# Performance work log

Hardware: AMD Instinct MI355X
Metric: run time of the kernel (lower is better)

The kernel has to match this reference:

```python
import jax, jax.numpy as jnp
import numpy as np

B, L, E, D = 4, 4096, 768, 64

def setup_inputs() -> dict:
    key = jax.random.key(0)
    ks = jax.random.split(key, 7)
    x = jax.random.normal(ks[0], (B, L, E), dtype=jnp.float32)
    # True = masked (strict upper triangle), as in masked_fill semantics
    causal_mask = jnp.triu(jnp.ones((L, L), dtype=bool), k=1)
    # True = valid token (inverted with ~ inside forward); all valid to avoid NaN rows
    pad_mask = jnp.ones((B, L), dtype=bool)
    s = 1.0 / np.sqrt(E)
    Wk = jax.random.uniform(ks[1], (E, D), jnp.float32, -s, s)
    bk = jax.random.uniform(ks[2], (D,), jnp.float32, -s, s)
    Wq = jax.random.uniform(ks[3], (E, D), jnp.float32, -s, s)
    bq = jax.random.uniform(ks[4], (D,), jnp.float32, -s, s)
    Wv = jax.random.uniform(ks[5], (E, D), jnp.float32, -s, s)
    bv = jax.random.uniform(ks[6], (D,), jnp.float32, -s, s)
    return {"x": x, "causal_mask": causal_mask, "pad_mask": pad_mask,
            "Wk": Wk, "bk": bk, "Wq": Wq, "bq": bq, "Wv": Wv, "bv": bv}

def reference(x, causal_mask, pad_mask, Wk, bk, Wq, bq, Wv, bv):
    # Linear projections: [B,L,E] @ [E,D] + [D]
    K = jnp.einsum('ble,ed->bld', x, Wk) + bk
    Q = jnp.einsum('ble,ed->bld', x, Wq) + bq
    V = jnp.einsum('ble,ed->bld', x, Wv) + bv
    d = Q.shape[-1]
    scores = jnp.einsum('bqd,bkd->bqk', Q, K) / jnp.sqrt(jnp.asarray(d, Q.dtype))
    # full_mask: causal (True=masked) OR key-position padding (~pad_mask, broadcast over query dim)
    full_mask = causal_mask[None, :, :] | (~pad_mask)[:, None, :]
    scores = jnp.where(full_mask, -jnp.inf, scores)
    attn = jax.nn.softmax(scores, axis=-1)
    out = jnp.einsum('bqk,bkd->bqd', attn, V)
    return out
```

## Files before the change

### kernel.cpp

```cpp
#include <hip/hip_runtime.h>

#define L_SEQ 4096
#define BATCH 4
#define EDIM 768

typedef __attribute__((ext_vector_type(8))) short bf16x8;
typedef __attribute__((ext_vector_type(4))) float f32x4;
typedef __attribute__((ext_vector_type(4))) unsigned short u16x4;
typedef __attribute__((ext_vector_type(8))) unsigned short u16x8;
typedef __attribute__((ext_vector_type(4))) _Float16 f16x4;
typedef __attribute__((ext_vector_type(8))) _Float16 f16x8;

__device__ __forceinline__ unsigned short f2bf(float f) {
  unsigned u = __builtin_bit_cast(unsigned, f);
  u += 0x7FFFu + ((u >> 16) & 1u);
  return (unsigned short)(u >> 16);
}

__global__ __launch_bounds__(256) void prep_kernel(
    const float* __restrict__ Wq, const float* __restrict__ Wk,
    const float* __restrict__ Wv, unsigned short* __restrict__ WT) {
  int g = blockIdx.x * 256 + threadIdx.x;
  if (g >= 192 * EDIM) return;
  int row = g / EDIM, k = g - row * EDIM;
  int z = row >> 6, n = row & 63;
  const float* W = (z == 0) ? Wq : (z == 1) ? Wk : Wv;
  WT[g] = f2bf(W[k * 64 + n]);
}

__global__ __launch_bounds__(256) void proj_kernel(
    const float* __restrict__ x, const unsigned short* __restrict__ WT,
    const float* __restrict__ bq, const float* __restrict__ bk, const float* __restrict__ bv,
    unsigned short* __restrict__ Qo, unsigned short* __restrict__ Kf,
    _Float16* __restrict__ Vf) {
  __shared__ unsigned short SH[2 * 13824];
  int tid = threadIdx.x;
  int w = tid >> 6, lane = tid & 63, l15 = lane & 15, g4 = lane >> 4;
  int m0 = blockIdx.x * 64;
  int brow = tid >> 3, bsg = tid & 7;

  f32x4 acc[3][4];
#pragma unroll
  for (int z = 0; z < 3; z++)
#pragma unroll
    for (int cf = 0; cf < 4; cf++) acc[z][cf] = (f32x4){0.f, 0.f, 0.f, 0.f};

  f32x4 arA[4], arB[4];
  u16x8 brA[6], brB[6];

  auto loadA = [&](f32x4 (&ar)[4], int k0) {
    const float* xp = x + (size_t)(m0 + 16 * w + l15) * EDIM + k0 + g4 * 8;
    ar[0] = *(const f32x4*)xp;
    ar[1] = *(const f32x4*)(xp + 4);
    ar[2] = *(const f32x4*)(xp + 32);
    ar[3] = *(const f32x4*)(xp + 36);
  };
  auto loadB = [&](u16x8 (&br)[6], int k0) {
#pragma unroll
    for (int pp = 0; pp < 6; pp++)
      br[pp] = *(const u16x8*)(WT + (size_t)(brow + pp * 32) * EDIM + k0 + bsg * 8);
  };
  auto writeB = [&](int cur, u16x8 (&br)[6]) {
#pragma unroll
    for (int pp = 0; pp < 6; pp++)
      *(u16x8*)&SH[cur * 13824 + (brow + pp * 32) * 72 + bsg * 8] = br[pp];
  };
  auto mkfrag = [&](f32x4 lo, f32x4 hi) {
    union { u16x8 u; bf16x8 b; } r;
    r.u[0] = f2bf(lo[0]); r.u[1] = f2bf(lo[1]); r.u[2] = f2bf(lo[2]); r.u[3] = f2bf(lo[3]);
    r.u[4] = f2bf(hi[0]); r.u[5] = f2bf(hi[1]); r.u[6] = f2bf(hi[2]); r.u[7] = f2bf(hi[3]);
    return r.b;
  };
  auto compute = [&](int cur, f32x4 (&ar)[4]) {
#pragma unroll
    for (int ks = 0; ks < 2; ks++) {
      bf16x8 a = mkfrag(ar[ks * 2], ar[ks * 2 + 1]);
#pragma unroll
      for (int z = 0; z < 3; z++)
#pragma unroll
        for (int cf = 0; cf < 4; cf++) {
          bf16x8 bb = *(const bf16x8*)&SH[cur * 13824 + (z * 64 + cf * 16 + l15) * 72 +
                                          ks * 32 + g4 * 8];
          acc[z][cf] = __builtin_amdgcn_mfma_f32_16x16x32_bf16(a, bb, acc[z][cf], 0, 0, 0);
        }
    }
  };

  loadA(arA, 0);
  loadB(brA, 0);
  for (int ss = 0; ss < 6; ss++) {
    int k1 = (2 * ss + 1) * 64;
    loadA(arB, k1);
    loadB(brB, k1);
    writeB(0, brA);
    __syncthreads();
    compute(0, arA);
    if (ss < 5) {
      int k2 = (2 * ss + 2) * 64;
      loadA(arA, k2);
      loadB(brA, k2);
    }
    writeB(1, brB);
    __syncthreads();
    compute(1, arB);
  }

  __syncthreads();
#pragma unroll
  for (int cf = 0; cf < 4; cf++) {
    int col = cf * 16 + l15;
    float bqv = bq[col], bkv = bk[col], bvv = bv[col];
#pragma unroll
    for (int r = 0; r < 4; r++) {
      int t = 16 * w + g4 * 4 + r;
      SH[t * 64 + col] = f2bf((acc[0][cf][r] + bqv) * 0.125f);
      int kidx = ((col >> 5) * 4 + (t >> 4)) * 512 +
                 (((col >> 3) & 3) * 16 + (t & 15)) * 8 + (col & 7);
      SH[4096 + kidx] = f2bf(acc[1][cf][r] + bkv);
      int vidx = ((t >> 4) * 2 + (col >> 5)) * 512 +
                 ((((t >> 2) & 3) * 16) + (col & 15)) * 8 + ((col >> 4) & 1) * 4 + (t & 3);
      _Float16 hv = (_Float16)(acc[2][cf][r] + bvv);
      SH[8192 + vidx] = *(unsigned short*)&hv;
    }
  }
  __syncthreads();
  {
    int b_ = m0 >> 12, jj = (m0 >> 6) & 63;
    size_t blk = (size_t)(b_ * 64 + jj) * 4096;
    const u16x8* s0 = (const u16x8*)&SH[tid * 16];
    u16x8* dq = (u16x8*)(Qo + (size_t)m0 * 64 + tid * 16);
    dq[0] = s0[0]; dq[1] = s0[1];
    const u16x8* s1 = (const u16x8*)&SH[4096 + tid * 16];
    u16x8* dk = (u16x8*)(Kf + blk + tid * 16);
    dk[0] = s1[0]; dk[1] = s1[1];
    const u16x8* s2 = (const u16x8*)&SH[8192 + tid * 16];
    u16x8* dv = (u16x8*)((unsigned short*)Vf + blk + tid * 16);
    dv[0] = s2[0]; dv[1] = s2[1];
  }
}

__global__ __launch_bounds__(256) void attn_kernel(
    const unsigned short* __restrict__ Qp, const unsigned short* __restrict__ Kf,
    const _Float16* __restrict__ Vf, float* __restrict__ out) {
  __shared__ float Ob[2][4][16][68];
  __shared__ float Ml[2][4][2][16];
  int tid = threadIdx.x;
  int p = tid >> 6, lane = tid & 63, l15 = lane & 15, g4 = lane >> 4;
  int flat = blockIdx.x;
  int xcd = flat & 7;
  int b = xcd >> 1;
  int pid = ((xcd & 1) << 6) + (flat >> 3);
  int sA = pid, sB = 255 - pid;
  size_t bL = (size_t)b * L_SEQ;

  const unsigned short* Kb = Kf + (size_t)b * 64 * 4096;
  const _Float16* Vb = Vf + (size_t)b * 64 * 4096;

  f32x4 o[4];
  float m, l;
  bf16x8 qf0, qf1;
  int qrow, jmax;

  auto loadkv = [&](bf16x8 (&kf)[8], f16x8 (&vp)[8], int j) {
    const unsigned short* kb = Kb + (size_t)j * 4096 + lane * 8;
    const _Float16* vb = Vb + (size_t)j * 4096 + lane * 8;
#pragma unroll
    for (int q = 0; q < 8; q++) kf[q] = *(const bf16x8*)(kb + q * 512);
#pragma unroll
    for (int q = 0; q < 8; q++) vp[q] = *(const f16x8*)(vb + q * 512);
  };

  auto step = [&](bf16x8 (&kf)[8], f16x8 (&vp)[8], int j) {
    f32x4 st[4];
#pragma unroll
    for (int i = 0; i < 4; i++) st[i] = (f32x4){0.f, 0.f, 0.f, 0.f};
    __builtin_amdgcn_s_setprio(1);
#pragma unroll
    for (int tb = 0; tb < 4; tb++)
      st[tb] = __builtin_amdgcn_mfma_f32_16x16x32_bf16(kf[tb], qf0, st[tb], 0, 0, 0);
#pragma unroll
    for (int tb = 0; tb < 4; tb++)
      st[tb] = __builtin_amdgcn_mfma_f32_16x16x32_bf16(kf[4 + tb], qf1, st[tb], 0, 0, 0);
    __builtin_amdgcn_s_setprio(0);

    if (j == jmax) {
#pragma unroll
      for (int tb = 0; tb < 4; tb++)
#pragma unroll
        for (int r = 0; r < 4; r++)
          if (j * 64 + tb * 16 + g4 * 4 + r > qrow) st[tb][r] = -1e30f;
    }

    float mx = st[0][0];
#pragma unroll
    for (int tb = 0; tb < 4; tb++)
#pragma unroll
      for (int r = 0; r < 4; r++) mx = fmaxf(mx, st[tb][r]);
    mx = fmaxf(mx, __shfl_xor(mx, 16));
    mx = fmaxf(mx, __shfl_xor(mx, 32));
    if (!__all(mx <= m + 8.0f)) {
      float mn = fmaxf(m, mx);
      float sc = __expf(m - mn);
      m = mn;
      l *= sc;
#pragma unroll
      for (int cf = 0; cf < 4; cf++)
#pragma unroll
        for (int r = 0; r < 4; r++) o[cf][r] *= sc;
    }
    float rs = 0.f;
#pragma unroll
    for (int tb = 0; tb < 4; tb++)
#pragma unroll
      for (int r = 0; r < 4; r++) { st[tb][r] = __expf(st[tb][r] - m); rs += st[tb][r]; }
    rs += __shfl_xor(rs, 16);
    rs += __shfl_xor(rs, 32);
    l += rs;

    f16x4 ph[4];
#pragma unroll
    for (int tb = 0; tb < 4; tb++) {
      ph[tb][0] = (_Float16)st[tb][0]; ph[tb][1] = (_Float16)st[tb][1];
      ph[tb][2] = (_Float16)st[tb][2]; ph[tb][3] = (_Float16)st[tb][3];
    }
    __builtin_amdgcn_s_setprio(1);
#pragma unroll
    for (int tb = 0; tb < 4; tb++) {
#pragma unroll
      for (int cf = 0; cf < 4; cf++) {
        f16x8 pr = vp[tb * 2 + (cf >> 1)];
        f16x4 va = (cf & 1) ? (f16x4){pr[4], pr[5], pr[6], pr[7]}
                            : (f16x4){pr[0], pr[1], pr[2], pr[3]};
        o[cf] = __builtin_amdgcn_mfma_f32_16x16x16f16(va, ph[tb], o[cf], 0, 0, 0);
      }
    }
    __builtin_amdgcn_s_setprio(0);
  };

  bf16x8 kfA[8], kfB[8];
  f16x8 vpA[8], vpB[8];

  auto run = [&](int s) {
    m = -1e38f; l = 0.f;
#pragma unroll
    for (int i = 0; i < 4; i++) o[i] = (f32x4){0.f, 0.f, 0.f, 0.f};
    qrow = s * 16 + l15;
    jmax = s >> 2;
    const unsigned short* Qb = Qp + (bL + qrow) * 64 + g4 * 8;
    qf0 = *(const bf16x8*)Qb;
    qf1 = *(const bf16x8*)(Qb + 32);
    int j = p;
    if (j > jmax) return;
    loadkv(kfA, vpA, j);
    while (true) {
      int jn = j + 4;
      bool hasB = (jn <= jmax);
      if (hasB) loadkv(kfB, vpB, jn);
      step(kfA, vpA, j);
      if (!hasB) break;
      j = jn;
      jn = j + 4;
      bool hasA = (jn <= jmax);
      if (hasA) loadkv(kfA, vpA, jn);
      step(kfB, vpB, j);
      if (!hasA) break;
      j = jn;
    }
  };

  auto stash = [&](int side) {
#pragma unroll
    for (int cf = 0; cf < 4; cf++)
      *(f32x4*)&Ob[side][p][l15][cf * 16 + g4 * 4] = o[cf];
    Ml[side][p][0][l15] = m;
    Ml[side][p][1][l15] = l;
  };

  run(sA); stash(0);
  run(sB); stash(1);
  __syncthreads();

  if (p < 2) {
    int s = p ? sB : sA;
    int q = lane >> 2, ch = lane & 3;
    float mw[4], lw[4];
#pragma unroll
    for (int w = 0; w < 4; w++) { mw[w] = Ml[p][w][0][q]; lw[w] = Ml[p][w][1][q]; }
    float ms = fmaxf(fmaxf(mw[0], mw[1]), fmaxf(mw[2], mw[3]));
    float ew[4]; float denom = 0.f;
#pragma unroll
    for (int w = 0; w < 4; w++) { ew[w] = __expf(mw[w] - ms); denom += lw[w] * ew[w]; }
    float inv = 1.0f / denom;
#pragma unroll
    for (int i = 0; i < 4; i++) {
      f32x4 acc = (f32x4){0.f, 0.f, 0.f, 0.f};
#pragma unroll
      for (int w = 0; w < 4; w++) {
        f32x4 v = *(const f32x4*)&Ob[p][w][q][ch * 16 + i * 4];
        acc += v * ew[w];
      }
      acc *= inv;
      *(f32x4*)(out + (bL + s * 16 + q) * 64 + ch * 16 + i * 4) = acc;
    }
  }
}

extern "C" void kernel_launch(void* const* d_in, const int* in_sizes, int n_in,
                              void* d_out, int out_size, void* d_ws, size_t ws_size,
                              hipStream_t stream) {
  const float* x  = (const float*)d_in[0];
  const float* Wk = (const float*)d_in[3];
  const float* bk = (const float*)d_in[4];
  const float* Wq = (const float*)d_in[5];
  const float* bq = (const float*)d_in[6];
  const float* Wv = (const float*)d_in[7];
  const float* bv = (const float*)d_in[8];
  float* out = (float*)d_out;

  char* ws = (char*)d_ws;
  unsigned short* WT = (unsigned short*)ws;
  unsigned short* Qo = (unsigned short*)(ws + 294912);
  unsigned short* Kf = (unsigned short*)(ws + 294912 + 2097152);
  _Float16*       Vf = (_Float16*)(ws + 294912 + 2 * 2097152);

  prep_kernel<<<576, 256, 0, stream>>>(Wq, Wk, Wv, WT);
  proj_kernel<<<256, 256, 0, stream>>>(x, WT, bq, bk, bv, Qo, Kf, Vf);
  attn_kernel<<<512, 256, 0, stream>>>(Qo, Kf, Vf, out);
}
```

Before: 53.89 us.

## Switch attention to 32x32 MFMA strips with shared K/V loads across paired query strips

Rewrites the attention kernel to use 32-row query strips with 32x32x16 bf16 and 32x32x8 f16 MFMAs, and changes the projection output layout to match. Each of 8 waves loads each K/V tile once and reuses it for both paired query strips, roughly halving K/V traffic per block. The launch moves to 256 blocks of 512 threads, and the cross-wave softmax merge now spans 8 waves. In exchange it carries more accumulator registers per wave and adds two block-wide reduction phases, which may limit occupancy.

```diff
diff --git a/kernel.cpp b/kernel.cpp
--- a/kernel.cpp
+++ b/kernel.cpp
@@ -6,15 +6,25 @@
 
 typedef __attribute__((ext_vector_type(8))) short bf16x8;
 typedef __attribute__((ext_vector_type(4))) float f32x4;
+typedef __attribute__((ext_vector_type(16))) float f32x16;
 typedef __attribute__((ext_vector_type(4))) unsigned short u16x4;
 typedef __attribute__((ext_vector_type(8))) unsigned short u16x8;
+typedef __attribute__((ext_vector_type(2))) _Float16 f16x2;
 typedef __attribute__((ext_vector_type(4))) _Float16 f16x4;
-typedef __attribute__((ext_vector_type(8))) _Float16 f16x8;
 
 __device__ __forceinline__ unsigned short f2bf(float f) {
   unsigned u = __builtin_bit_cast(unsigned, f);
   u += 0x7FFFu + ((u >> 16) & 1u);
   return (unsigned short)(u >> 16);
+}
+
+__device__ __forceinline__ f16x4 half_of(u16x8 v, int h) {
+  u16x4 t = h ? (u16x4){v[4], v[5], v[6], v[7]} : (u16x4){v[0], v[1], v[2], v[3]};
+  return __builtin_bit_cast(f16x4, t);
+}
+
+__device__ __forceinline__ f16x2 pkrtz(float a, float b) {
+  return __builtin_bit_cast(f16x2, __builtin_amdgcn_cvt_pkrtz(a, b));
 }
 
 __global__ __launch_bounds__(256) void prep_kernel(
@@ -31,8 +41,8 @@
 __global__ __launch_bounds__(256) void proj_kernel(
     const float* __restrict__ x, const unsigned short* __restrict__ WT,
     const float* __restrict__ bq, const float* __restrict__ bk, const float* __restrict__ bv,
-    unsigned short* __restrict__ Qo, unsigned short* __restrict__ Kf,
-    _Float16* __restrict__ Vf) {
+    unsigned short* __restrict__ Qf, unsigned short* __restrict__ Kf,
+    unsigned short* __restrict__ Vf) {
   __shared__ unsigned short SH[2 * 13824];
   int tid = threadIdx.x;
   int w = tid >> 6, lane = tid & 63, l15 = lane & 15, g4 = lane >> 4;
@@ -106,203 +116,194 @@
   }
 
   __syncthreads();
+  unsigned short* LQ = SH;
+  unsigned short* LK = SH + 4096;
+  unsigned short* LV = SH + 8192;
 #pragma unroll
   for (int cf = 0; cf < 4; cf++) {
-    int col = cf * 16 + l15;
-    float bqv = bq[col], bkv = bk[col], bvv = bv[col];
+    int d = cf * 16 + l15;
+    float bqv = bq[d], bkv = bk[d], bvv = bv[d];
 #pragma unroll
     for (int r = 0; r < 4; r++) {
       int t = 16 * w + g4 * 4 + r;
-      SH[t * 64 + col] = f2bf((acc[0][cf][r] + bqv) * 0.125f);
-      int kidx = ((col >> 5) * 4 + (t >> 4)) * 512 +
-                 (((col >> 3) & 3) * 16 + (t & 15)) * 8 + (col & 7);
-      SH[4096 + kidx] = f2bf(acc[1][cf][r] + bkv);
-      int vidx = ((t >> 4) * 2 + (col >> 5)) * 512 +
-                 ((((t >> 2) & 3) * 16) + (col & 15)) * 8 + ((col >> 4) & 1) * 4 + (t & 3);
+      int sl = t >> 5, tl = t & 31;
+      int fqk = sl * 2048 + (d >> 4) * 512 + (tl + ((d >> 3) & 1) * 32) * 8 + (d & 7);
+      LQ[fqk] = f2bf((acc[0][cf][r] + bqv) * 0.125f);
+      LK[fqk] = f2bf(acc[1][cf][r] + bkv);
+      int fv = sl * 2048 + (d >> 5) * 1024 + ((tl >> 4) & 1) * 512 +
+               ((d & 31) + ((tl >> 2) & 1) * 32) * 8 + ((tl >> 3) & 1) * 4 + (tl & 3);
       _Float16 hv = (_Float16)(acc[2][cf][r] + bvv);
-      SH[8192 + vidx] = *(unsigned short*)&hv;
+      LV[fv] = __builtin_bit_cast(unsigned short, hv);
     }
   }
   __syncthreads();
   {
-    int b_ = m0 >> 12, jj = (m0 >> 6) & 63;
-    size_t blk = (size_t)(b_ * 64 + jj) * 4096;
-    const u16x8* s0 = (const u16x8*)&SH[tid * 16];
-    u16x8* dq = (u16x8*)(Qo + (size_t)m0 * 64 + tid * 16);
-    dq[0] = s0[0]; dq[1] = s0[1];
-    const u16x8* s1 = (const u16x8*)&SH[4096 + tid * 16];
-    u16x8* dk = (u16x8*)(Kf + blk + tid * 16);
-    dk[0] = s1[0]; dk[1] = s1[1];
-    const u16x8* s2 = (const u16x8*)&SH[8192 + tid * 16];
-    u16x8* dv = (u16x8*)((unsigned short*)Vf + blk + tid * 16);
-    dv[0] = s2[0]; dv[1] = s2[1];
-  }
-}
-
-__global__ __launch_bounds__(256) void attn_kernel(
-    const unsigned short* __restrict__ Qp, const unsigned short* __restrict__ Kf,
-    const _Float16* __restrict__ Vf, float* __restrict__ out) {
-  __shared__ float Ob[2][4][16][68];
-  __shared__ float Ml[2][4][2][16];
+    int bb = m0 >> 12;
+    int S0 = (m0 >> 5) & 127;
+    size_t base = ((size_t)(bb * 128 + S0)) * 2048;
+    u16x8* dq = (u16x8*)(Qf + base);
+    u16x8* dk = (u16x8*)(Kf + base);
+    u16x8* dv = (u16x8*)(Vf + base);
+    const u16x8* sq = (const u16x8*)LQ;
+    const u16x8* sk = (const u16x8*)LK;
+    const u16x8* sv = (const u16x8*)LV;
+    dq[tid * 2] = sq[tid * 2]; dq[tid * 2 + 1] = sq[tid * 2 + 1];
+    dk[tid * 2] = sk[tid * 2]; dk[tid * 2 + 1] = sk[tid * 2 + 1];
+    dv[tid * 2] = sv[tid * 2]; dv[tid * 2 + 1] = sv[tid * 2 + 1];
+  }
+}
+
+__global__ __launch_bounds__(512, 2) void attn_kernel(
+    const unsigned short* __restrict__ Qf, const unsigned short* __restrict__ Kf,
+    const unsigned short* __restrict__ Vf, float* __restrict__ out) {
+  __shared__ float OB[8][32][68];
+  __shared__ float ML[8][2][32];
   int tid = threadIdx.x;
-  int p = tid >> 6, lane = tid & 63, l15 = lane & 15, g4 = lane >> 4;
-  int flat = blockIdx.x;
-  int xcd = flat & 7;
+  int w = tid >> 6, lane = tid & 63;
+  int ql = lane & 31, hi = lane >> 5;
+  int blk = blockIdx.x;
+  int xcd = blk & 7;
   int b = xcd >> 1;
-  int pid = ((xcd & 1) << 6) + (flat >> 3);
-  int sA = pid, sB = 255 - pid;
+  int pid = ((xcd & 1) << 5) | (blk >> 3);
+  int sA = pid, sB = 127 - pid;
   size_t bL = (size_t)b * L_SEQ;
-
-  const unsigned short* Kb = Kf + (size_t)b * 64 * 4096;
-  const _Float16* Vb = Vf + (size_t)b * 64 * 4096;
-
-  f32x4 o[4];
-  float m, l;
-  bf16x8 qf0, qf1;
-  int qrow, jmax;
-
-  auto loadkv = [&](bf16x8 (&kf)[8], f16x8 (&vp)[8], int j) {
-    const unsigned short* kb = Kb + (size_t)j * 4096 + lane * 8;
-    const _Float16* vb = Vb + (size_t)j * 4096 + lane * 8;
-#pragma unroll
-    for (int q = 0; q < 8; q++) kf[q] = *(const bf16x8*)(kb + q * 512);
-#pragma unroll
-    for (int q = 0; q < 8; q++) vp[q] = *(const f16x8*)(vb + q * 512);
-  };
-
-  auto step = [&](bf16x8 (&kf)[8], f16x8 (&vp)[8], int j) {
-    f32x4 st[4];
-#pragma unroll
-    for (int i = 0; i < 4; i++) st[i] = (f32x4){0.f, 0.f, 0.f, 0.f};
+  const unsigned short* Qb = Qf + (size_t)b * 128 * 2048;
+  const unsigned short* Kb = Kf + (size_t)b * 128 * 2048;
+  const unsigned short* Vb = Vf + (size_t)b * 128 * 2048;
+
+  bf16x8 qA[4], qB[4];
+#pragma unroll
+  for (int kh = 0; kh < 4; kh++) {
+    qA[kh] = *(const bf16x8*)(Qb + ((size_t)sA * 4 + kh) * 512 + lane * 8);
+    qB[kh] = *(const bf16x8*)(Qb + ((size_t)sB * 4 + kh) * 512 + lane * 8);
+  }
+  f32x16 oA0, oA1, oB0, oB1;
+#pragma unroll
+  for (int i = 0; i < 16; i++) { oA0[i] = 0.f; oA1[i] = 0.f; oB0[i] = 0.f; oB1[i] = 0.f; }
+  float mA = -1e38f, lA = 0.f, mB = -1e38f, lB = 0.f;
+
+  auto loadKV = [&](bf16x8 (&kf)[4], u16x8 (&vf)[4], int j) {
+    const unsigned short* kp = Kb + (size_t)j * 2048 + lane * 8;
+    const unsigned short* vp = Vb + (size_t)j * 2048 + lane * 8;
+#pragma unroll
+    for (int q = 0; q < 4; q++) kf[q] = *(const bf16x8*)(kp + q * 512);
+#pragma unroll
+    for (int q = 0; q < 4; q++) vf[q] = *(const u16x8*)(vp + q * 512);
+  };
+
+  auto strip = [&](bf16x8 (&kf)[4], u16x8 (&vf)[4], int j, int s, bf16x8 (&qf)[4],
+                   f32x16& o0, f32x16& o1, float& m, float& l) {
+    f32x16 st;
+#pragma unroll
+    for (int i = 0; i < 16; i++) st[i] = 0.f;
     __builtin_amdgcn_s_setprio(1);
 #pragma unroll
-    for (int tb = 0; tb < 4; tb++)
-      st[tb] = __builtin_amdgcn_mfma_f32_16x16x32_bf16(kf[tb], qf0, st[tb], 0, 0, 0);
-#pragma unroll
-    for (int tb = 0; tb < 4; tb++)
-      st[tb] = __builtin_amdgcn_mfma_f32_16x16x32_bf16(kf[4 + tb], qf1, st[tb], 0, 0, 0);
+    for (int kh = 0; kh < 4; kh++)
+      st = __builtin_amdgcn_mfma_f32_32x32x16_bf16(kf[kh], qf[kh], st, 0, 0, 0);
     __builtin_amdgcn_s_setprio(0);
 
-    if (j == jmax) {
-#pragma unroll
-      for (int tb = 0; tb < 4; tb++)
-#pragma unroll
-        for (int r = 0; r < 4; r++)
-          if (j * 64 + tb * 16 + g4 * 4 + r > qrow) st[tb][r] = -1e30f;
-    }
-
-    float mx = st[0][0];
-#pragma unroll
-    for (int tb = 0; tb < 4; tb++)
-#pragma unroll
-      for (int r = 0; r < 4; r++) mx = fmaxf(mx, st[tb][r]);
-    mx = fmaxf(mx, __shfl_xor(mx, 16));
+    if (j == s) {
+#pragma unroll
+      for (int r = 0; r < 16; r++) {
+        int tl = (r & 3) + 8 * (r >> 2) + 4 * hi;
+        if (tl > ql) st[r] = -1e30f;
+      }
+    }
+
+    float mx = st[0];
+#pragma unroll
+    for (int r = 1; r < 16; r++) mx = fmaxf(mx, st[r]);
     mx = fmaxf(mx, __shfl_xor(mx, 32));
     if (!__all(mx <= m + 8.0f)) {
       float mn = fmaxf(m, mx);
       float sc = __expf(m - mn);
-      m = mn;
-      l *= sc;
-#pragma unroll
-      for (int cf = 0; cf < 4; cf++)
-#pragma unroll
-        for (int r = 0; r < 4; r++) o[cf][r] *= sc;
+      m = mn; l *= sc;
+#pragma unroll
+      for (int i = 0; i < 16; i++) { o0[i] *= sc; o1[i] *= sc; }
     }
     float rs = 0.f;
 #pragma unroll
-    for (int tb = 0; tb < 4; tb++)
-#pragma unroll
-      for (int r = 0; r < 4; r++) { st[tb][r] = __expf(st[tb][r] - m); rs += st[tb][r]; }
-    rs += __shfl_xor(rs, 16);
+    for (int r = 0; r < 16; r++) { st[r] = __expf(st[r] - m); rs += st[r]; }
     rs += __shfl_xor(rs, 32);
     l += rs;
 
-    f16x4 ph[4];
-#pragma unroll
-    for (int tb = 0; tb < 4; tb++) {
-      ph[tb][0] = (_Float16)st[tb][0]; ph[tb][1] = (_Float16)st[tb][1];
-      ph[tb][2] = (_Float16)st[tb][2]; ph[tb][3] = (_Float16)st[tb][3];
+    f16x4 pb[4];
+#pragma unroll
+    for (int oc = 0; oc < 4; oc++) {
+      f16x2 a = pkrtz(st[4 * oc], st[4 * oc + 1]);
+      f16x2 c = pkrtz(st[4 * oc + 2], st[4 * oc + 3]);
+      pb[oc] = (f16x4){a[0], a[1], c[0], c[1]};
     }
     __builtin_amdgcn_s_setprio(1);
 #pragma unroll
-    for (int tb = 0; tb < 4; tb++) {
-#pragma unroll
-      for (int cf = 0; cf < 4; cf++) {
-        f16x8 pr = vp[tb * 2 + (cf >> 1)];
-        f16x4 va = (cf & 1) ? (f16x4){pr[4], pr[5], pr[6], pr[7]}
-                            : (f16x4){pr[0], pr[1], pr[2], pr[3]};
-        o[cf] = __builtin_amdgcn_mfma_f32_16x16x16f16(va, ph[tb], o[cf], 0, 0, 0);
-      }
-    }
+    for (int oc = 0; oc < 4; oc++)
+      o0 = __builtin_amdgcn_mfma_f32_32x32x8f16(half_of(vf[oc >> 1], oc & 1), pb[oc], o0, 0, 0, 0);
+#pragma unroll
+    for (int oc = 0; oc < 4; oc++)
+      o1 = __builtin_amdgcn_mfma_f32_32x32x8f16(half_of(vf[2 + (oc >> 1)], oc & 1), pb[oc], o1, 0, 0, 0);
     __builtin_amdgcn_s_setprio(0);
   };
 
-  bf16x8 kfA[8], kfB[8];
-  f16x8 vpA[8], vpB[8];
-
-  auto run = [&](int s) {
-    m = -1e38f; l = 0.f;
-#pragma unroll
-    for (int i = 0; i < 4; i++) o[i] = (f32x4){0.f, 0.f, 0.f, 0.f};
-    qrow = s * 16 + l15;
-    jmax = s >> 2;
-    const unsigned short* Qb = Qp + (bL + qrow) * 64 + g4 * 8;
-    qf0 = *(const bf16x8*)Qb;
-    qf1 = *(const bf16x8*)(Qb + 32);
-    int j = p;
-    if (j > jmax) return;
-    loadkv(kfA, vpA, j);
+  auto step = [&](bf16x8 (&kf)[4], u16x8 (&vf)[4], int j) {
+    if (j <= sA) strip(kf, vf, j, sA, qA, oA0, oA1, mA, lA);
+    strip(kf, vf, j, sB, qB, oB0, oB1, mB, lB);
+  };
+
+  bf16x8 kfA[4], kfB[4];
+  u16x8 vfA[4], vfB[4];
+  {
+    int j = w;
+    loadKV(kfA, vfA, j);
     while (true) {
-      int jn = j + 4;
-      bool hasB = (jn <= jmax);
-      if (hasB) loadkv(kfB, vpB, jn);
-      step(kfA, vpA, j);
+      int jn = j + 8;
+      bool hasB = (jn <= sB);
+      if (hasB) loadKV(kfB, vfB, jn);
+      step(kfA, vfA, j);
       if (!hasB) break;
       j = jn;
-      jn = j + 4;
-      bool hasA = (jn <= jmax);
-      if (hasA) loadkv(kfA, vpA, jn);
-      step(kfB, vpB, j);
+      jn = j + 8;
+      bool hasA = (jn <= sB);
+      if (hasA) loadKV(kfA, vfA, jn);
+      step(kfB, vfB, j);
       if (!hasA) break;
       j = jn;
     }
-  };
-
-  auto stash = [&](int side) {
-#pragma unroll
-    for (int cf = 0; cf < 4; cf++)
-      *(f32x4*)&Ob[side][p][l15][cf * 16 + g4 * 4] = o[cf];
-    Ml[side][p][0][l15] = m;
-    Ml[side][p][1][l15] = l;
-  };
-
-  run(sA); stash(0);
-  run(sB); stash(1);
-  __syncthreads();
-
-  if (p < 2) {
-    int s = p ? sB : sA;
-    int q = lane >> 2, ch = lane & 3;
-    float mw[4], lw[4];
-#pragma unroll
-    for (int w = 0; w < 4; w++) { mw[w] = Ml[p][w][0][q]; lw[w] = Ml[p][w][1][q]; }
-    float ms = fmaxf(fmaxf(mw[0], mw[1]), fmaxf(mw[2], mw[3]));
-    float ew[4]; float denom = 0.f;
-#pragma unroll
-    for (int w = 0; w < 4; w++) { ew[w] = __expf(mw[w] - ms); denom += lw[w] * ew[w]; }
+  }
+
+  auto stash_reduce = [&](int s, f32x16& o0, f32x16& o1, float m, float l) {
+    __syncthreads();
+#pragma unroll
+    for (int g = 0; g < 4; g++) {
+      *(f32x4*)&OB[w][ql][8 * g + 4 * hi] =
+          (f32x4){o0[4 * g], o0[4 * g + 1], o0[4 * g + 2], o0[4 * g + 3]};
+      *(f32x4*)&OB[w][ql][32 + 8 * g + 4 * hi] =
+          (f32x4){o1[4 * g], o1[4 * g + 1], o1[4 * g + 2], o1[4 * g + 3]};
+    }
+    if (hi == 0) { ML[w][0][ql] = m; ML[w][1][ql] = l; }
+    __syncthreads();
+    int q = tid >> 4, dg = tid & 15;
+    float mw[8], lw[8];
+    float ms = -1e38f;
+#pragma unroll
+    for (int ww = 0; ww < 8; ww++) {
+      mw[ww] = ML[ww][0][q]; lw[ww] = ML[ww][1][q];
+      ms = fmaxf(ms, mw[ww]);
+    }
+    float denom = 0.f, ew[8];
+#pragma unroll
+    for (int ww = 0; ww < 8; ww++) { ew[ww] = __expf(mw[ww] - ms); denom += lw[ww] * ew[ww]; }
     float inv = 1.0f / denom;
-#pragma unroll
-    for (int i = 0; i < 4; i++) {
-      f32x4 acc = (f32x4){0.f, 0.f, 0.f, 0.f};
-#pragma unroll
-      for (int w = 0; w < 4; w++) {
-        f32x4 v = *(const f32x4*)&Ob[p][w][q][ch * 16 + i * 4];
-        acc += v * ew[w];
-      }
-      acc *= inv;
-      *(f32x4*)(out + (bL + s * 16 + q) * 64 + ch * 16 + i * 4) = acc;
-    }
-  }
+    f32x4 acc = (f32x4){0.f, 0.f, 0.f, 0.f};
+#pragma unroll
+    for (int ww = 0; ww < 8; ww++) {
+      f32x4 v = *(const f32x4*)&OB[ww][q][dg * 4];
+      acc += v * ew[ww];
+    }
+    acc *= inv;
+    *(f32x4*)(out + (bL + (size_t)s * 32 + q) * 64 + dg * 4) = acc;
+  };
+  stash_reduce(sA, oA0, oA1, mA, lA);
+  stash_reduce(sB, oB0, oB1, mB, lB);
 }
 
 extern "C" void kernel_launch(void* const* d_in, const int* in_sizes, int n_in,
@@ -319,11 +320,11 @@
 
   char* ws = (char*)d_ws;
   unsigned short* WT = (unsigned short*)ws;
-  unsigned short* Qo = (unsigned short*)(ws + 294912);
+  unsigned short* Qf = (unsigned short*)(ws + 294912);
   unsigned short* Kf = (unsigned short*)(ws + 294912 + 2097152);
-  _Float16*       Vf = (_Float16*)(ws + 294912 + 2 * 2097152);
+  unsigned short* Vf = (unsigned short*)(ws + 294912 + 2 * 2097152);
 
   prep_kernel<<<576, 256, 0, stream>>>(Wq, Wk, Wv, WT);
-  proj_kernel<<<256, 256, 0, stream>>>(x, WT, bq, bk, bv, Qo, Kf, Vf);
-  attn_kernel<<<512, 256, 0, stream>>>(Qo, Kf, Vf, out);
-}
+  proj_kernel<<<256, 256, 0, stream>>>(x, WT, bq, bk, bv, Qf, Kf, Vf);
+  attn_kernel<<<256, 512, 0, stream>>>(Qf, Kf, Vf, out);
+}
```

After: 48.13 us. 1.12x faster.
